# Kernel tuning notes

Measured on AMD Instinct MI355X. Metric: run time of the kernel, lower is better.

Reference implementation:

```python
import jax, jax.numpy as jnp
import numpy as np

H, W = 1024, 2048
K_CENTERS = 32          # fixed-size stand-in for torch.nonzero(center_heatmap > 0)
ROAD_ID = 0             # cityscapes trainId for 'road'
THING_START = 11        # cityscapes thing classes are trainIds >= 11
LABEL_DIVISOR = 1000
FILTER_IDS = (10, 19)   # 'sky', 'ego vehicle' depth filter classes
EPS = 1e-8


def _group_instances(heat, off, sem):
    # heat: (H,W) f32, off: (2,H,W) f32 [dy,dx], sem: (1,H,W) int
    vals, idx = jax.lax.top_k(heat.reshape(-1), K_CENTERS)
    cy = (idx // W).astype(jnp.float32)
    cx = (idx % W).astype(jnp.float32)
    valid = vals > 0.0
    ys = jnp.arange(H, dtype=jnp.float32)[:, None] + off[0]   # (H,W)
    xs = jnp.arange(W, dtype=jnp.float32)[None, :] + off[1]   # (H,W)
    d2 = (ys[None] - cy[:, None, None]) ** 2 + (xs[None] - cx[:, None, None]) ** 2  # (K,H,W)
    d2 = jnp.where(valid[:, None, None], d2, jnp.inf)
    inst = (jnp.argmin(d2, axis=0) + 1).astype(sem.dtype)     # (H,W), 1-based instance ids
    thing = sem >= THING_START
    any_valid = jnp.any(valid)
    return jnp.where(thing & any_valid, sem * LABEL_DIVISOR + inst[None], sem)


def _surface_normal(p):
    # p: (1,3,H,W) camera-space points; central-difference cross-product stencil
    px = jnp.pad(p, ((0, 0), (0, 0), (0, 0), (1, 1)), mode='edge')
    py = jnp.pad(p, ((0, 0), (0, 0), (1, 1), (0, 0)), mode='edge')
    vx = px[:, :, :, 2:] - px[:, :, :, :-2]
    vy = py[:, :, 2:, :] - py[:, :, :-2, :]
    n = jnp.cross(vx, vy, axis=1)
    return n / (jnp.linalg.norm(n, axis=1, keepdims=True) + EPS)


def setup_inputs() -> dict:
    key = jax.random.key(0)
    k1, k2, k3, k4 = jax.random.split(key, 4)
    sem_seg = jax.random.randint(k1, (1, 1, H, W), 0, 19, dtype=jnp.int64)
    center_heatmap = jax.random.normal(k2, (1, 1, H, W), dtype=jnp.float32) - 3.0
    offsets = jax.random.normal(k3, (1, 2, H, W), dtype=jnp.float32) * 5.0
    depth_logits = jax.random.uniform(k4, (1, 1, H, W), dtype=jnp.float32, minval=0.5, maxval=80.0)
    K_mat = np.array([[2262.52, 0.0, 1096.98], [0.0, 2265.30, 513.14], [0.0, 0.0, 1.0]], dtype=np.float32)
    inverse_camera_matrix = jnp.asarray(np.linalg.inv(K_mat), dtype=jnp.float32)
    real_camera_height = jnp.ones((1,), dtype=jnp.float32) * 1.7
    return {"sem_seg": sem_seg, "center_heatmap": center_heatmap, "offsets": offsets,
            "depth_logits": depth_logits, "inverse_camera_matrix": inverse_camera_matrix,
            "real_camera_height": real_camera_height}


def reference(sem_seg, center_heatmap, offsets, depth_logits, inverse_camera_matrix, real_camera_height):
    sem = sem_seg[0]                       # (1,H,W) int
    sem = _group_instances(center_heatmap[0, 0], offsets[0], sem)
    # pixel grid -> normalized camera rays
    xm = jnp.broadcast_to(jnp.arange(W, dtype=jnp.float32)[None, :], (H, W))
    ym = jnp.broadcast_to(jnp.arange(H, dtype=jnp.float32)[:, None], (H, W))
    grid = jnp.stack([xm, ym, jnp.ones((H, W), jnp.float32)], axis=0)           # (3,H,W)
    xnorm = jnp.einsum('ij,jhw->ihw', inverse_camera_matrix, grid)[None]        # (1,3,H,W)
    cam_points = xnorm * depth_logits                                           # (1,3,H,W)
    ground = sem == ROAD_ID                                                     # (1,H,W)
    normal = _surface_normal(cam_points)
    cam_heights = jnp.abs(jnp.sum(cam_points * normal, axis=1))                 # (1,H,W)
    # masked lower-median (torch.median semantics): sort with inf padding
    vals = jnp.where(ground, cam_heights, jnp.inf).reshape(-1)
    cnt = jnp.sum(ground.astype(jnp.int32))
    med_idx = jnp.maximum((cnt - 1) // 2, 0)
    cam_height = jnp.sort(vals)[med_idx]
    scale = real_camera_height.reshape(()) / cam_height
    depth = depth_logits * scale
    cam_points = cam_points * scale
    filt = (sem == FILTER_IDS[0])
    for cid in FILTER_IDS[1:]:
        filt = filt | (sem == cid)
    depth = jnp.where(filt[:, None], 0.0, depth)                                # (1,1,H,W)
    cam_out = jnp.concatenate([cam_points[0], sem.astype(jnp.float32)], axis=0).transpose(1, 2, 0)  # (H,W,4)
    return sem.astype(jnp.int32), depth[0], cam_out
```

## Files before the change

kernel.cpp:

```cpp
#include <hip/hip_runtime.h>
#include <math.h>

#define HH 1024
#define WW 2048
#define HW (HH*WW)
#define KC 32
#define LCAP 6144
#define CREG 16
#define KCAP 12288
#define SENT 0xFFFFFFFFu
#define BIAS 16777216.0f

typedef unsigned long long u64;

struct Scratch {
  unsigned hist0[2048];
  unsigned hist1[2048];
  unsigned hist2[2048];
  unsigned done0;
  int nvalid;
  float scale;
  float ck[KC], m2cy[KC], m2cx[KC];
  unsigned ccnt[2048];
  unsigned cblk[2048];
};

__device__ __forceinline__ unsigned agent_load(const unsigned* p){
  return __hip_atomic_load(p, __ATOMIC_RELAXED, __HIP_MEMORY_SCOPE_AGENT);
}

template<int CTRL>
__device__ __forceinline__ u64 dpp_mov64(u64 x){
  unsigned lo = (unsigned)x, hi = (unsigned)(x>>32);
  unsigned nlo = (unsigned)__builtin_amdgcn_update_dpp((int)lo, (int)lo, CTRL, 0xF, 0xF, false);
  unsigned nhi = (unsigned)__builtin_amdgcn_update_dpp((int)hi, (int)hi, CTRL, 0xF, 0xF, false);
  return ((u64)nhi<<32) | (u64)nlo;
}
__device__ __forceinline__ u64 wave_max64(u64 x){
  u64 y;
  y = dpp_mov64<0x111>(x); if (y > x) x = y;
  y = dpp_mov64<0x112>(x); if (y > x) x = y;
  y = dpp_mov64<0x114>(x); if (y > x) x = y;
  y = dpp_mov64<0x118>(x); if (y > x) x = y;
  y = dpp_mov64<0x142>(x); if (y > x) x = y;
  y = dpp_mov64<0x143>(x); if (y > x) x = y;
  unsigned mlo = (unsigned)__builtin_amdgcn_readlane((int)(unsigned)x, 63);
  unsigned mhi = (unsigned)__builtin_amdgcn_readlane((int)(unsigned)(x>>32), 63);
  return ((u64)mhi<<32) | (u64)mlo;
}

__device__ __forceinline__ void grid_bar(unsigned* ctr, unsigned target){
  __syncthreads();
  if (threadIdx.x == 0){
    atomicAdd(ctr, 1u);
    while (__hip_atomic_load(ctr, __ATOMIC_RELAXED, __HIP_MEMORY_SCOPE_AGENT) < target)
      __builtin_amdgcn_s_sleep(2);
  }
  __syncthreads();
}

template<int PASS>
__device__ __forceinline__ void pick512(const unsigned* gh, unsigned* wsumL, unsigned* res){
  int t = threadIdx.x;
  unsigned v0 = agent_load(&gh[t*4+0]);
  unsigned v1 = agent_load(&gh[t*4+1]);
  unsigned v2 = agent_load(&gh[t*4+2]);
  unsigned v3 = agent_load(&gh[t*4+3]);
  int kin_prev = (PASS==0) ? 0 : (int)res[1];
  unsigned s = v0+v1+v2+v3;
  unsigned incl = s;
  #pragma unroll
  for (int d=1; d<64; d<<=1){ unsigned o = __shfl_up(incl, d); if ((t&63) >= d) incl += o; }
  unsigned excl = incl - s;
  if ((t&63)==63) wsumL[t>>6] = incl;
  __syncthreads();
  unsigned woff=0, total=0;
  #pragma unroll
  for (int w=0;w<8;w++){ unsigned xw=wsumL[w]; if (w < (t>>6)) woff += xw; total += xw; }
  unsigned pre = woff + excl;
  int k = (PASS==0) ? ((total>0) ? (int)((total-1)>>1) : 0) : kin_prev;
  if (total>0 && (unsigned)k >= pre && (unsigned)k < pre + s){
    unsigned kr = (unsigned)k - pre;
    int b_ = t*4;
    if (kr >= v0){ kr -= v0; b_++;
      if (kr >= v1){ kr -= v1; b_++;
        if (kr >= v2){ kr -= v2; b_++; } } }
    res[0] = (unsigned)b_; res[1] = kr;
  }
  if (t==0) res[2] = total;
  __syncthreads();
}

__global__ __launch_bounds__(256) void kA(const float* __restrict__ heat,
    const int* __restrict__ sem, const float* __restrict__ depth,
    const float* __restrict__ invK, u64* __restrict__ cand,
    unsigned* __restrict__ cheight, Scratch* __restrict__ sc){
  __shared__ unsigned wc_c[4], wc_g[4];
  int t = threadIdx.x;
  if (blockIdx.x == 0){
    unsigned* hz = sc->hist0;
    for (int j=t; j<6144; j+=256) hz[j] = 0u;
    if (t==0) sc->done0 = 0u;
  }
  int i4 = blockIdx.x*256 + t;
  int p = i4<<2;
  int y = p>>11, x = p&2047;
  int row = y<<11;

  float4 hq = ((const float4*)heat)[i4];
  int4   s4 = ((const int4*)sem)[i4];
  float4 dc = ((const float4*)depth)[i4];
  float  dl = depth[row + (x>0 ? x-1 : 0)];
  float  dr = depth[row + (x+4<WW ? x+4 : WW-1)];
  int rowu = (y>0)?    row-WW : row;
  int rowd = (y<HH-1)? row+WW : row;
  float4 du = ((const float4*)(depth + rowu))[x>>2];
  float4 dd = ((const float4*)(depth + rowd))[x>>2];
  float ik0=invK[0],ik1=invK[1],ik2=invK[2];
  float ik3=invK[3],ik4=invK[4],ik5=invK[5];
  float ik6=invK[6],ik7=invK[7],ik8=invK[8];

  float hv[4] = {hq.x,hq.y,hq.z,hq.w};
  int   sv[4] = {s4.x,s4.y,s4.z,s4.w};
  float dcv[4]= {dc.x,dc.y,dc.z,dc.w};
  float duv[4]= {du.x,du.y,du.z,du.w};
  float ddv[4]= {dd.x,dd.y,dd.z,dd.w};

  unsigned npos = 0, ng = 0;
  #pragma unroll
  for (int j=0;j<4;j++){ npos += (hv[j] > 0.0f) ? 1u : 0u; ng += (sv[j]==0) ? 1u : 0u; }
  unsigned incc = npos, incg = ng;
  #pragma unroll
  for (int d=1; d<64; d<<=1){
    unsigned oc = __shfl_up(incc, d), og = __shfl_up(incg, d);
    if ((t&63) >= d){ incc += oc; incg += og; }
  }
  if ((t&63)==63){ wc_c[t>>6] = incc; wc_g[t>>6] = incg; }

  float fy = (float)y;
  float a0=ik1*fy+ik2, a1=ik4*fy+ik5, a2=ik7*fy+ik8;
  float fyu=(y>0)?    fy-1.0f : fy;
  float fyd=(y<HH-1)? fy+1.0f : fy;
  float uu0=ik1*fyu+ik2, uu1=ik4*fyu+ik5, uu2=ik7*fyu+ik8;
  float ww0=ik1*fyd+ik2, ww1=ik4*fyd+ik5, ww2=ik7*fyd+ik8;
  float dxmv[4] = {dl, dcv[0], dcv[1], dcv[2]};
  float dxpv[4] = {dcv[1], dcv[2], dcv[3], dr};
  float h[4];
  #pragma unroll
  for (int j=0;j<4;j++){
    float fx  = (float)(x+j);
    float fxm = (x+j>0)?    fx-1.0f : fx;
    float fxp = (x+j<WW-1)? fx+1.0f : fx;
    float pc0=(ik0*fx +a0)*dcv[j],  pc1=(ik3*fx +a1)*dcv[j],  pc2=(ik6*fx +a2)*dcv[j];
    float pm0=(ik0*fxm+a0)*dxmv[j], pm1=(ik3*fxm+a1)*dxmv[j], pm2=(ik6*fxm+a2)*dxmv[j];
    float pp0=(ik0*fxp+a0)*dxpv[j], pp1=(ik3*fxp+a1)*dxpv[j], pp2=(ik6*fxp+a2)*dxpv[j];
    float pu0=(ik0*fx+uu0)*duv[j],  pu1=(ik3*fx+uu1)*duv[j],  pu2=(ik6*fx+uu2)*duv[j];
    float pd0=(ik0*fx+ww0)*ddv[j],  pd1=(ik3*fx+ww1)*ddv[j],  pd2=(ik6*fx+ww2)*ddv[j];
    float vx0=pp0-pm0, vx1=pp1-pm1, vx2=pp2-pm2;
    float vy0=pd0-pu0, vy1=pd1-pu1, vy2=pd2-pu2;
    float n0=vx1*vy2-vx2*vy1, n1=vx2*vy0-vx0*vy2, n2=vx0*vy1-vx1*vy0;
    float nn = sqrtf(n0*n0+n1*n1+n2*n2) + 1e-8f;
    h[j] = fabsf(pc0*n0+pc1*n1+pc2*n2) / nn;
  }

  __syncthreads();
  unsigned cboff=0, gboff=0;
  int myw = t>>6;
  #pragma unroll
  for (int w=0;w<4;w++){
    if (w < myw){ cboff += wc_c[w]; gboff += wc_g[w]; }
  }
  if (npos){
    unsigned cslot = cboff + incc - npos;
    u64* cb = cand + ((size_t)blockIdx.x * CREG);
    #pragma unroll
    for (int j=0;j<4;j++){
      if (hv[j] > 0.0f){
        if (cslot < CREG)
          cb[cslot] = ((u64)__float_as_uint(hv[j])<<32) | (u64)(unsigned)(~(unsigned)(p+j));
        cslot++;
      }
    }
  }
  if (ng){
    unsigned gslot = ((unsigned)blockIdx.x<<10) + gboff + incg - ng;
    #pragma unroll
    for (int j=0;j<4;j++){
      if (sv[j]==0){ cheight[gslot++] = __float_as_uint(h[j]); }
    }
  }
  if (t==0){
    unsigned tc = wc_c[0]+wc_c[1]+wc_c[2]+wc_c[3];
    sc->ccnt[blockIdx.x] = (tc > CREG) ? CREG : tc;
    sc->cblk[blockIdx.x] = wc_g[0]+wc_g[1]+wc_g[2]+wc_g[3];
  }
}

__global__ __launch_bounds__(512) void k_med(const unsigned* __restrict__ ch,
    const u64* __restrict__ cand, Scratch* __restrict__ sc,
    const float* __restrict__ rch){
  __shared__ union {
    struct { unsigned keys[KCAP]; } med;
    struct { u64 lcache[LCAP]; u64 loc[8*KC]; } sel;
  } u;
  __shared__ unsigned hsh[2048];
  __shared__ unsigned wsumL[8];
  __shared__ unsigned res[3];
  __shared__ unsigned cnts[32];
  __shared__ unsigned rstart[32];
  __shared__ unsigned misc[2];
  __shared__ unsigned stot;
  int t = threadIdx.x;
  int b = blockIdx.x;
  int lane = t & 63;
  int w = t >> 6;

  if (b == 64){
    if (t==0) stot = 0u;
    if (t < 8*KC) u.sel.loc[t] = 0ULL;
    __syncthreads();
    #pragma unroll
    for (int rep=0; rep<4; rep++){
      int r = t + rep*512;
      unsigned c = sc->ccnt[r];
      if (c){
        unsigned bpos = atomicAdd(&stot, c);
        const u64* cb = cand + ((size_t)r * CREG);
        for (unsigned i=0;i<c;i++){
          unsigned pos = bpos+i;
          if (pos < LCAP) u.sel.lcache[pos] = cb[i];
        }
      }
    }
    __syncthreads();
    int n = (int)stot; if (n > LCAP) n = LCAP;
    int chunk = (n + 7) >> 3;
    int start = w * chunk;
    int end   = min(n, start + chunk);
    u64 c0,c1,c2,c3,c4,c5,c6,c7;
    {
      int b0 = start + lane;
      c0 = (b0     < end) ? u.sel.lcache[b0]     : 0ULL;
      c1 = (b0+64  < end) ? u.sel.lcache[b0+64]  : 0ULL;
      c2 = (b0+128 < end) ? u.sel.lcache[b0+128] : 0ULL;
      c3 = (b0+192 < end) ? u.sel.lcache[b0+192] : 0ULL;
      c4 = (b0+256 < end) ? u.sel.lcache[b0+256] : 0ULL;
      c5 = (b0+320 < end) ? u.sel.lcache[b0+320] : 0ULL;
      c6 = (b0+384 < end) ? u.sel.lcache[b0+384] : 0ULL;
      c7 = (b0+448 < end) ? u.sel.lcache[b0+448] : 0ULL;
    }
    bool over = (end - start) > 512;
    u64 prev = ~0ULL;
    for (int r=0;r<KC;r++){
      u64 best = 0ULL;
      if (c0 < prev && c0 > best) best = c0;
      if (c1 < prev && c1 > best) best = c1;
      if (c2 < prev && c2 > best) best = c2;
      if (c3 < prev && c3 > best) best = c3;
      if (c4 < prev && c4 > best) best = c4;
      if (c5 < prev && c5 > best) best = c5;
      if (c6 < prev && c6 > best) best = c6;
      if (c7 < prev && c7 > best) best = c7;
      if (over){
        for (int idx = start + 512 + lane; idx < end; idx += 64){
          u64 kk = u.sel.lcache[idx];
          if (kk < prev && kk > best) best = kk;
        }
      }
      u64 m = wave_max64(best);
      if (m == 0ULL) break;
      if (lane == 0) u.sel.loc[w*KC + r] = m;
      prev = m;
    }
    __syncthreads();
    if (w == 0){
      int p2 = 0;
      u64 key2 = (lane < 8) ? u.sel.loc[lane*KC] : 0ULL;
      int k = 0;
      for (int r=0;r<KC;r++){
        u64 m = wave_max64(key2);
        if (m == 0ULL) break;
        if (lane == 0){
          unsigned idx = ~(unsigned)(m & 0xFFFFFFFFULL);
          float cy = (float)(idx >> 11), cx = (float)(idx & 2047u);
          sc->ck[r]   = cy*cy + cx*cx + BIAS;
          sc->m2cy[r] = -2.0f*cy;
          sc->m2cx[r] = -2.0f*cx;
        }
        u64 ball = __ballot(key2 == m);
        int winner = __ffsll((long long)ball) - 1;
        if (lane == winner){
          p2++;
          key2 = (p2 < KC) ? u.sel.loc[lane*KC + p2] : 0ULL;
        }
        k = r + 1;
      }
      if (lane == 0) sc->nvalid = k;
    }
    return;
  }

  int r0 = b * 32;
  if (t < 32) cnts[t] = sc->cblk[r0+t];
  if (t == 0){ res[0]=0u; res[1]=0u; res[2]=0u; }
  for (int j=t;j<2048;j+=512) hsh[j]=0u;
  __syncthreads();
  if (t == 0){
    unsigned acc=0, ov=0;
    for (int r=0;r<32;r++){
      unsigned c = cnts[r];
      if (acc + c <= KCAP){ rstart[r] = acc; acc += c; }
      else { rstart[r] = 0xFFFFFFFFu; ov |= (1u<<r); }
    }
    misc[0] = acc; misc[1] = ov;
  }
  __syncthreads();
  unsigned ldsn = misc[0], ovmask = misc[1];
  for (int r=0;r<32;r++){
    unsigned rs = rstart[r];
    if (rs != 0xFFFFFFFFu){
      unsigned c = cnts[r];
      const unsigned* base = ch + ((size_t)(r0+r)<<10);
      for (unsigned i=t; i<c; i+=512) u.med.keys[rs+i] = base[i];
    }
  }
  __syncthreads();

  for (unsigned i=t; i<ldsn; i+=512) atomicAdd(&hsh[u.med.keys[i]>>21], 1u);
  {
    unsigned ovm = ovmask;
    while (ovm){
      int r = __ffs(ovm)-1; ovm &= ovm-1;
      unsigned c = cnts[r];
      const unsigned* base = ch + ((size_t)(r0+r)<<10);
      for (unsigned i=t; i<c; i+=512) atomicAdd(&hsh[base[i]>>21], 1u);
    }
  }
  __syncthreads();
  for (int j=t;j<2048;j+=512){ unsigned v=hsh[j]; if (v) atomicAdd(&sc->hist0[j], v); }
  grid_bar(&sc->done0, 64);
  pick512<0>(sc->hist0, wsumL, res);
  unsigned tot0 = res[2];
  unsigned pref0 = res[0];
  for (int j=t;j<2048;j+=512) hsh[j]=0u;
  __syncthreads();

  for (unsigned i=t; i<ldsn; i+=512){
    unsigned key = u.med.keys[i];
    if ((key>>21) == pref0) atomicAdd(&hsh[(key>>10)&2047u], 1u);
  }
  {
    unsigned ovm = ovmask;
    while (ovm){
      int r = __ffs(ovm)-1; ovm &= ovm-1;
      unsigned c = cnts[r];
      const unsigned* base = ch + ((size_t)(r0+r)<<10);
      for (unsigned i=t; i<c; i+=512){
        unsigned key = base[i];
        if ((key>>21) == pref0) atomicAdd(&hsh[(key>>10)&2047u], 1u);
      }
    }
  }
  __syncthreads();
  for (int j=t;j<2048;j+=512){ unsigned v=hsh[j]; if (v) atomicAdd(&sc->hist1[j], v); }
  grid_bar(&sc->done0, 128);
  pick512<1>(sc->hist1, wsumL, res);
  unsigned pref01 = (pref0 << 11) | res[0];
  for (int j=t;j<2048;j+=512) hsh[j]=0u;
  __syncthreads();

  for (unsigned i=t; i<ldsn; i+=512){
    unsigned key = u.med.keys[i];
    if ((key>>10) == pref01) atomicAdd(&hsh[key & 1023u], 1u);
  }
  {
    unsigned ovm = ovmask;
    while (ovm){
      int r = __ffs(ovm)-1; ovm &= ovm-1;
      unsigned c = cnts[r];
      const unsigned* base = ch + ((size_t)(r0+r)<<10);
      for (unsigned i=t; i<c; i+=512){
        unsigned key = base[i];
        if ((key>>10) == pref01) atomicAdd(&hsh[key & 1023u], 1u);
      }
    }
  }
  __syncthreads();
  for (int j=t;j<2048;j+=512){ unsigned v=hsh[j]; if (v) atomicAdd(&sc->hist2[j], v); }
  grid_bar(&sc->done0, 192);
  pick512<2>(sc->hist2, wsumL, res);
  if (b == 0 && t == 0){
    unsigned key = (pref01 << 10) | res[0];
    sc->scale = (tot0 > 0) ? (rch[0] / __uint_as_float(key)) : 0.0f;
  }
}

__global__ __launch_bounds__(256) void k_final(const int* __restrict__ sem,
    const float* __restrict__ off, const float* __restrict__ depth,
    const float* __restrict__ invK, const Scratch* __restrict__ sc,
    float* __restrict__ out){
  __shared__ float sck[KC], smy[KC], smx[KC];
  __shared__ int snv; __shared__ float ssc;
  int t = threadIdx.x;
  if (t < KC){ sck[t]=sc->ck[t]; smy[t]=sc->m2cy[t]; smx[t]=sc->m2cx[t]; }
  if (t == 0){ snv = sc->nvalid; ssc = sc->scale; }
  __syncthreads();

  int i4 = blockIdx.x*256 + t;
  int p = i4<<2;
  int y = p>>11, x = p&2047;
  int4   s4 = ((const int4*)sem)[i4];
  float4 oy = ((const float4*)off)[i4];
  float4 ox = ((const float4*)(off+HW))[i4];
  float4 dc = ((const float4*)depth)[i4];

  float ik0=invK[0],ik1=invK[1],ik2=invK[2];
  float ik3=invK[3],ik4=invK[4],ik5=invK[5];
  float ik6=invK[6],ik7=invK[7],ik8=invK[8];
  float fy = (float)y;
  float a0=ik1*fy+ik2, a1=ik4*fy+ik5, a2=ik7*fy+ik8;
  int nv = snv; float s = ssc;

  int   sv[4]  = {s4.x,s4.y,s4.z,s4.w};
  float oyv[4] = {oy.x,oy.y,oy.z,oy.w};
  float oxv[4] = {ox.x,ox.y,ox.z,ox.w};
  float dv[4]  = {dc.x,dc.y,dc.z,dc.w};

  float ys[4], xs[4]; unsigned ub[4];
  #pragma unroll
  for (int j=0;j<4;j++){
    ys[j] = fy + oyv[j]; xs[j] = (float)(x+j) + oxv[j]; ub[j] = SENT;
  }
  for (int k=0;k<nv;k++){
    float ckk=sck[k], my=smy[k], mx=smx[k];
    #pragma unroll
    for (int j=0;j<4;j++){
      float tt = fmaf(ys[j], my, ckk);
      tt = fmaf(xs[j], mx, tt);
      unsigned uu = (__float_as_uint(tt) & ~31u) | (unsigned)k;
      ub[j] = uu < ub[j] ? uu : ub[j];
    }
  }
  float lab[4], depo[4];
  float4* cam = (float4*)(out + (size_t)2*HW);
  #pragma unroll
  for (int j=0;j<4;j++){
    int sj = sv[j];
    lab[j] = (sj >= 11 && nv > 0) ? (float)(sj*1000 + (int)(ub[j]&31u) + 1) : (float)sj;
    float fx = (float)(x+j);
    float ds = dv[j]*s;
    float p0=(ik0*fx+a0)*ds, p1=(ik3*fx+a1)*ds, p2=(ik6*fx+a2)*ds;
    bool filt = (lab[j]==10.0f) || (lab[j]==19.0f);
    depo[j] = filt ? 0.0f : ds;
    cam[p+j] = make_float4(p0, p1, p2, lab[j]);
  }
  ((float4*)out)[i4]      = make_float4(lab[0], lab[1], lab[2], lab[3]);
  ((float4*)(out+HW))[i4] = make_float4(depo[0], depo[1], depo[2], depo[3]);
}

extern "C" void kernel_launch(void* const* d_in, const int* in_sizes, int n_in,
                              void* d_out, int out_size, void* d_ws, size_t ws_size,
                              hipStream_t stream){
  const int*   sem   = (const int*)d_in[0];
  const float* heat  = (const float*)d_in[1];
  const float* off   = (const float*)d_in[2];
  const float* depth = (const float*)d_in[3];
  const float* invK  = (const float*)d_in[4];
  const float* rch   = (const float*)d_in[5];
  float* out = (float*)d_out;

  unsigned* cheight = (unsigned*)d_ws;
  u64* cand = (u64*)((char*)d_ws + (size_t)HW*4);
  Scratch* sc = (Scratch*)((char*)d_ws + (size_t)HW*4 + (size_t)2048*CREG*8);

  const int grid4 = HW/4/256;

  kA<<<grid4, 256, 0, stream>>>(heat, sem, depth, invK, cand, cheight, sc);
  k_med<<<65, 512, 0, stream>>>(cheight, cand, sc, rch);
  k_final<<<grid4, 256, 0, stream>>>(sem, off, depth, invK, sc, out);
}
```

Before: 67.57 us.

## Compact ground heights and candidates per wavefront instead of per block

The producer kernel now compacts ground-pixel heights and heatmap candidates per 64-lane wavefront, which removes the shared-memory cross-wave prefix and the block-wide barrier. Output regions become 8192 per-wave segments of 256 heights and 8 candidate slots. The median kernel no longer stages keys into LDS. Each of its 64 blocks scans 128 wave segments straight from global memory with masked strided loops in all three radix passes. This re-reads global memory three times, walks padded slots, and caps candidates at 8 per wave, which could drop true top-k centers in dense regions.

```diff
diff --git a/kernel.cpp b/kernel.cpp
--- a/kernel.cpp
+++ b/kernel.cpp
@@ -6,8 +6,8 @@
 #define HW (HH*WW)
 #define KC 32
 #define LCAP 6144
-#define CREG 16
-#define KCAP 12288
+#define NW 8192
+#define CREGW 8
 #define SENT 0xFFFFFFFFu
 #define BIAS 16777216.0f
 
@@ -21,8 +21,8 @@
   int nvalid;
   float scale;
   float ck[KC], m2cy[KC], m2cx[KC];
-  unsigned ccnt[2048];
-  unsigned cblk[2048];
+  unsigned ccnt[NW];
+  unsigned cblk[NW];
 };
 
 __device__ __forceinline__ unsigned agent_load(const unsigned* p){
@@ -95,7 +95,6 @@
     const int* __restrict__ sem, const float* __restrict__ depth,
     const float* __restrict__ invK, u64* __restrict__ cand,
     unsigned* __restrict__ cheight, Scratch* __restrict__ sc){
-  __shared__ unsigned wc_c[4], wc_g[4];
   int t = threadIdx.x;
   if (blockIdx.x == 0){
     unsigned* hz = sc->hist0;
@@ -106,6 +105,8 @@
   int p = i4<<2;
   int y = p>>11, x = p&2047;
   int row = y<<11;
+  int lane = t & 63;
+  unsigned wid = (unsigned)(blockIdx.x*4 + (t>>6));
 
   float4 hq = ((const float4*)heat)[i4];
   int4   s4 = ((const int4*)sem)[i4];
@@ -133,9 +134,8 @@
   #pragma unroll
   for (int d=1; d<64; d<<=1){
     unsigned oc = __shfl_up(incc, d), og = __shfl_up(incg, d);
-    if ((t&63) >= d){ incc += oc; incg += og; }
-  }
-  if ((t&63)==63){ wc_c[t>>6] = incc; wc_g[t>>6] = incg; }
+    if (lane >= d){ incc += oc; incg += og; }
+  }
 
   float fy = (float)y;
   float a0=ik1*fy+ik2, a1=ik4*fy+ik5, a2=ik7*fy+ik8;
@@ -163,36 +163,28 @@
     h[j] = fabsf(pc0*n0+pc1*n1+pc2*n2) / nn;
   }
 
-  __syncthreads();
-  unsigned cboff=0, gboff=0;
-  int myw = t>>6;
-  #pragma unroll
-  for (int w=0;w<4;w++){
-    if (w < myw){ cboff += wc_c[w]; gboff += wc_g[w]; }
-  }
   if (npos){
-    unsigned cslot = cboff + incc - npos;
-    u64* cb = cand + ((size_t)blockIdx.x * CREG);
+    unsigned cslot = incc - npos;
+    u64* cb = cand + ((size_t)wid * CREGW);
     #pragma unroll
     for (int j=0;j<4;j++){
       if (hv[j] > 0.0f){
-        if (cslot < CREG)
+        if (cslot < CREGW)
           cb[cslot] = ((u64)__float_as_uint(hv[j])<<32) | (u64)(unsigned)(~(unsigned)(p+j));
         cslot++;
       }
     }
   }
   if (ng){
-    unsigned gslot = ((unsigned)blockIdx.x<<10) + gboff + incg - ng;
+    unsigned gslot = (wid<<8) + (incg - ng);
     #pragma unroll
     for (int j=0;j<4;j++){
       if (sv[j]==0){ cheight[gslot++] = __float_as_uint(h[j]); }
     }
   }
-  if (t==0){
-    unsigned tc = wc_c[0]+wc_c[1]+wc_c[2]+wc_c[3];
-    sc->ccnt[blockIdx.x] = (tc > CREG) ? CREG : tc;
-    sc->cblk[blockIdx.x] = wc_g[0]+wc_g[1]+wc_g[2]+wc_g[3];
+  if (lane == 63){
+    sc->ccnt[wid] = (incc > CREGW) ? CREGW : incc;
+    sc->cblk[wid] = incg;
   }
 }
 
@@ -200,15 +192,12 @@
     const u64* __restrict__ cand, Scratch* __restrict__ sc,
     const float* __restrict__ rch){
   __shared__ union {
-    struct { unsigned keys[KCAP]; } med;
+    struct { unsigned cnts[128]; } med;
     struct { u64 lcache[LCAP]; u64 loc[8*KC]; } sel;
   } u;
   __shared__ unsigned hsh[2048];
   __shared__ unsigned wsumL[8];
   __shared__ unsigned res[3];
-  __shared__ unsigned cnts[32];
-  __shared__ unsigned rstart[32];
-  __shared__ unsigned misc[2];
   __shared__ unsigned stot;
   int t = threadIdx.x;
   int b = blockIdx.x;
@@ -220,12 +209,12 @@
     if (t < 8*KC) u.sel.loc[t] = 0ULL;
     __syncthreads();
     #pragma unroll
-    for (int rep=0; rep<4; rep++){
+    for (int rep=0; rep<16; rep++){
       int r = t + rep*512;
       unsigned c = sc->ccnt[r];
       if (c){
         unsigned bpos = atomicAdd(&stot, c);
-        const u64* cb = cand + ((size_t)r * CREG);
+        const u64* cb = cand + ((size_t)r * CREGW);
         for (unsigned i=0;i<c;i++){
           unsigned pos = bpos+i;
           if (pos < LCAP) u.sel.lcache[pos] = cb[i];
@@ -300,41 +289,15 @@
     return;
   }
 
-  int r0 = b * 32;
-  if (t < 32) cnts[t] = sc->cblk[r0+t];
+  int r0 = b * 128;
+  const unsigned* chb = ch + ((size_t)r0 << 8);
+  if (t < 128) u.med.cnts[t] = sc->cblk[r0 + t];
   if (t == 0){ res[0]=0u; res[1]=0u; res[2]=0u; }
   for (int j=t;j<2048;j+=512) hsh[j]=0u;
   __syncthreads();
-  if (t == 0){
-    unsigned acc=0, ov=0;
-    for (int r=0;r<32;r++){
-      unsigned c = cnts[r];
-      if (acc + c <= KCAP){ rstart[r] = acc; acc += c; }
-      else { rstart[r] = 0xFFFFFFFFu; ov |= (1u<<r); }
-    }
-    misc[0] = acc; misc[1] = ov;
-  }
-  __syncthreads();
-  unsigned ldsn = misc[0], ovmask = misc[1];
-  for (int r=0;r<32;r++){
-    unsigned rs = rstart[r];
-    if (rs != 0xFFFFFFFFu){
-      unsigned c = cnts[r];
-      const unsigned* base = ch + ((size_t)(r0+r)<<10);
-      for (unsigned i=t; i<c; i+=512) u.med.keys[rs+i] = base[i];
-    }
-  }
-  __syncthreads();
-
-  for (unsigned i=t; i<ldsn; i+=512) atomicAdd(&hsh[u.med.keys[i]>>21], 1u);
-  {
-    unsigned ovm = ovmask;
-    while (ovm){
-      int r = __ffs(ovm)-1; ovm &= ovm-1;
-      unsigned c = cnts[r];
-      const unsigned* base = ch + ((size_t)(r0+r)<<10);
-      for (unsigned i=t; i<c; i+=512) atomicAdd(&hsh[base[i]>>21], 1u);
-    }
+
+  for (unsigned e=t; e<128*256; e+=512){
+    if ((e & 255u) < u.med.cnts[e>>8]) atomicAdd(&hsh[chb[e]>>21], 1u);
   }
   __syncthreads();
   for (int j=t;j<2048;j+=512){ unsigned v=hsh[j]; if (v) atomicAdd(&sc->hist0[j], v); }
@@ -345,20 +308,10 @@
   for (int j=t;j<2048;j+=512) hsh[j]=0u;
   __syncthreads();
 
-  for (unsigned i=t; i<ldsn; i+=512){
-    unsigned key = u.med.keys[i];
-    if ((key>>21) == pref0) atomicAdd(&hsh[(key>>10)&2047u], 1u);
-  }
-  {
-    unsigned ovm = ovmask;
-    while (ovm){
-      int r = __ffs(ovm)-1; ovm &= ovm-1;
-      unsigned c = cnts[r];
-      const unsigned* base = ch + ((size_t)(r0+r)<<10);
-      for (unsigned i=t; i<c; i+=512){
-        unsigned key = base[i];
-        if ((key>>21) == pref0) atomicAdd(&hsh[(key>>10)&2047u], 1u);
-      }
+  for (unsigned e=t; e<128*256; e+=512){
+    if ((e & 255u) < u.med.cnts[e>>8]){
+      unsigned key = chb[e];
+      if ((key>>21) == pref0) atomicAdd(&hsh[(key>>10)&2047u], 1u);
     }
   }
   __syncthreads();
@@ -369,20 +322,10 @@
   for (int j=t;j<2048;j+=512) hsh[j]=0u;
   __syncthreads();
 
-  for (unsigned i=t; i<ldsn; i+=512){
-    unsigned key = u.med.keys[i];
-    if ((key>>10) == pref01) atomicAdd(&hsh[key & 1023u], 1u);
-  }
-  {
-    unsigned ovm = ovmask;
-    while (ovm){
-      int r = __ffs(ovm)-1; ovm &= ovm-1;
-      unsigned c = cnts[r];
-      const unsigned* base = ch + ((size_t)(r0+r)<<10);
-      for (unsigned i=t; i<c; i+=512){
-        unsigned key = base[i];
-        if ((key>>10) == pref01) atomicAdd(&hsh[key & 1023u], 1u);
-      }
+  for (unsigned e=t; e<128*256; e+=512){
+    if ((e & 255u) < u.med.cnts[e>>8]){
+      unsigned key = chb[e];
+      if ((key>>10) == pref01) atomicAdd(&hsh[key & 1023u], 1u);
     }
   }
   __syncthreads();
@@ -470,8 +413,8 @@
   float* out = (float*)d_out;
 
   unsigned* cheight = (unsigned*)d_ws;
-  u64* cand = (u64*)((char*)d_ws + (size_t)HW*4);
-  Scratch* sc = (Scratch*)((char*)d_ws + (size_t)HW*4 + (size_t)2048*CREG*8);
+  u64* cand = (u64*)((char*)d_ws + (size_t)NW*256*4);
+  Scratch* sc = (Scratch*)((char*)d_ws + (size_t)NW*256*4 + (size_t)NW*CREGW*8);
 
   const int grid4 = HW/4/256;
 
```

New measurement: 88.23 us. 30.6% more time.
